# Optimization experiments

Measured on AMD Instinct MI355X. Metric: run time of the kernel, lower is better.

Reference implementation:

```python
import jax, jax.numpy as jnp
import numpy as np

ATT_WIDTH = 512  # attention_width from init

def _band_mask(T, width, dtype):
    # tf.matrix_band_part(ones, width//2, (width-1)//2): keep i-j<=lower and j-i<=upper
    lower = width // 2
    upper = (width - 1) // 2
    i = jnp.arange(T)[:, None]
    j = jnp.arange(T)[None, :]
    keep = (i - j <= lower) & (j - i <= upper)
    return keep.astype(dtype)

def setup_inputs() -> dict:
    key = jax.random.key(0)
    k1, k2, k3, k4 = jax.random.split(key, 4)
    B, T, H, D = 8, 2048, 1024, 1024
    scale = 1.0 / np.sqrt(H)  # keep activations sane
    return {
        "inputs": jax.random.normal(k1, (B, T, H), dtype=jnp.float32),
        "WQ": jax.random.normal(k2, (H, D), dtype=jnp.float32) * scale,
        "WK": jax.random.normal(k3, (H, D), dtype=jnp.float32) * scale,
        "WV": jax.random.normal(k4, (H, D), dtype=jnp.float32) * scale,
    }

def reference(inputs, WQ, WK, WV) -> jnp.ndarray:
    B, T, H = inputs.shape
    D = WQ.shape[1]
    scale = jnp.asarray(D, inputs.dtype) ** 0.5
    q = jnp.einsum('bth,hd->btd', inputs, WQ)
    k = jnp.einsum('bth,hd->btd', inputs, WK)
    v = jnp.einsum('bth,hd->btd', inputs, WV)
    score = jnp.einsum('bqd,bkd->bqk', q, k) / scale  # [B,T,T]
    # NOTE: original multiplies score by the 0/1 band mask BEFORE softmax
    # (masked entries become 0, not -inf). Faithful reproduction.
    local = _band_mask(T, ATT_WIDTH, score.dtype)
    score = score * local[None, :, :]
    attn = jax.nn.softmax(score, axis=-1)
    return jnp.einsum('bqk,bkd->bqd', attn, v)
```

## Files before the change

kernel.cpp:

```cpp
#include <hip/hip_runtime.h>
#include <hip/hip_bf16.h>
#include <stdint.h>

typedef __attribute__((ext_vector_type(8))) short bf16x8;
typedef __attribute__((ext_vector_type(4))) short short4v;
typedef __attribute__((ext_vector_type(4))) float f32x4;

#define DEV static __device__ __forceinline__

DEV float bf2f(short u) {
    union { float f; uint32_t i; } c; c.i = ((uint32_t)(uint16_t)u) << 16; return c.f;
}
DEV short f2bf(float f) {
    union { float f; uint32_t i; } c; c.f = f;
    uint32_t i = c.i;
    uint32_t r = i + 0x7FFFu + ((i >> 16) & 1u);
    return (short)(r >> 16);
}

DEV void gload_lds16(const short* g, short* l) {
    __builtin_amdgcn_global_load_lds(
        (const __attribute__((address_space(1))) void*)g,
        (__attribute__((address_space(3))) void*)l,
        16, 0, 0);
}

__global__ __launch_bounds__(256)
void cvt_f32_bf16(const float* __restrict__ in, short* __restrict__ out) {
    long i = ((long)blockIdx.x * 256 + threadIdx.x) * 8;
    float4 a = *(const float4*)&in[i];
    float4 b = *(const float4*)&in[i + 4];
    bf16x8 o;
    o[0] = f2bf(a.x); o[1] = f2bf(a.y); o[2] = f2bf(a.z); o[3] = f2bf(a.w);
    o[4] = f2bf(b.x); o[5] = f2bf(b.y); o[6] = f2bf(b.z); o[7] = f2bf(b.w);
    *(bf16x8*)&out[i] = o;
}

__global__ __launch_bounds__(256)
void transpose_w(const float* __restrict__ W, short* __restrict__ Wt) {
    const int HD = 1024;
    __shared__ float tile[32][33];
    int bx = blockIdx.x, by = blockIdx.y;
    int tx = threadIdx.x & 31, ty = threadIdx.x >> 5;
    #pragma unroll
    for (int r = ty; r < 32; r += 8)
        tile[r][tx] = W[(long)(by * 32 + r) * HD + bx * 32 + tx];
    __syncthreads();
    #pragma unroll
    for (int r = ty; r < 32; r += 8)
        Wt[(long)(bx * 32 + r) * HD + by * 32 + tx] = f2bf(tile[tx][r]);
}


DEV void stage_half(const short* __restrict__ src, int ld, short* dst, int tid) {
    int rr = tid >> 3;
    int cs = ((tid & 7) ^ (rr & 7)) << 3;
    short* d = dst + ((tid >> 6) << 9);
    gload_lds16(src + (long)rr * ld + cs, d);
    gload_lds16(src + (long)(rr + 64) * ld + cs, d + 4096);
}

DEV bf16x8 ld_frag(const short* half, int rowbase, int ks, int lane) {
    int row = rowbase + (lane & 15);
    int idx = (row << 6) + ks * 32 + ((lane >> 4) << 3);
    idx ^= (lane & 7) << 3;
    return *(const bf16x8*)&half[idx];
}

#define SCHED0 __builtin_amdgcn_sched_barrier(0)
#define SBAR do { SCHED0; __builtin_amdgcn_s_barrier(); SCHED0; } while (0)
#define LGK(n) do { asm volatile("s_waitcnt lgkmcnt(" #n ")" ::: "memory"); SCHED0; } while (0)
#define VM(n)  do { asm volatile("s_waitcnt vmcnt(" #n ")" ::: "memory"); SCHED0; } while (0)
#define PRIO1 __builtin_amdgcn_s_setprio(1)
#define PRIO0 __builtin_amdgcn_s_setprio(0)

#define READ_A(HP, QM)                                                          \
    do { _Pragma("unroll") for (int iq = 0; iq < 4; ++iq)                       \
         _Pragma("unroll") for (int ks = 0; ks < 2; ++ks)                       \
             ra[iq][ks] = ld_frag(HP, (QM)*64 + iq*16, ks, lane); } while (0)

#define READ_B(HP, QN)                                                          \
    do { _Pragma("unroll") for (int jn = 0; jn < 2; ++jn)                       \
         _Pragma("unroll") for (int ks = 0; ks < 2; ++ks)                       \
             rb[QN][jn][ks] = ld_frag(HP, wn1*64 + (QN)*32 + jn*16, ks, lane); } while (0)

#define MFMA_Q(QM, QN)                                                          \
    do { _Pragma("unroll") for (int iq = 0; iq < 4; ++iq)                       \
         _Pragma("unroll") for (int jn = 0; jn < 2; ++jn)                       \
         _Pragma("unroll") for (int ks = 0; ks < 2; ++ks)                       \
             acc[(QM)*4+iq][(QN)*2+jn] = __builtin_amdgcn_mfma_f32_16x16x32_bf16( \
                 ra[iq][ks], rb[QN][jn][ks], acc[(QM)*4+iq][(QN)*2+jn], 0,0,0); } while (0)

template<int EPI>
__global__ __launch_bounds__(512, 2)
void gemm256(const short* __restrict__ Abase, const short* __restrict__ Bbase,
             void* __restrict__ o0, void* __restrict__ o1, void* __restrict__ o2,
             const float* __restrict__ Crow, const float* __restrict__ Vsum)
{
    const int T = 2048, HD = 1024;
    __shared__ __align__(16) short lds[2][2][2][8192];

    const int tid  = threadIdx.x;
    const int lane = tid & 63;
    const int w    = tid >> 6;
    const int wm   = w >> 2;
    const int wn   = w & 3;
    const int wn1  = wn & 1;

    int m0, n0, klo, khi, ldA, ldB, bz;
    const short *A, *B;
    if (EPI == 0) {
        int p = (int)blockIdx.x + 12 * (int)blockIdx.y;
        int lid = (p & 7) * 96 + (p >> 3);
        m0 = (lid / 12) * 256; n0 = (lid % 12) * 256;
        klo = 0; khi = 1024; ldA = HD; ldB = HD; bz = 0;
        A = Abase; B = Bbase;
    } else if (EPI == 1) {
        int p = (int)blockIdx.x + 3 * ((int)blockIdx.y + 8 * (int)blockIdx.z);
        bz = p & 7; int rem = p >> 3;
        int mb = rem / 3, kb = mb + rem % 3 - 1;
        if (kb < 0 || kb > 7) return;
        m0 = mb * 256; n0 = kb * 256;
        klo = 0; khi = 1024; ldA = HD; ldB = HD;
        A = Abase + (long)bz * T * HD; B = Bbase + (long)bz * T * HD;
    } else {
        int p = (int)blockIdx.x + 4 * ((int)blockIdx.y + 8 * (int)blockIdx.z);
        bz = p & 7; int rem = p >> 3;
        int mb = rem / 4;
        m0 = mb * 256; n0 = (rem % 4) * 256;
        klo = max(m0 - 256, 0); khi = min(m0 + 512, T);
        ldA = T; ldB = T;
        A = Abase + (long)bz * T * T; B = Bbase + (long)bz * HD * T;
    }

    const short* Asrc = A + (long)m0 * ldA + klo;
    const short* Bsrc = B + (long)n0 * ldB + klo;
    const short* hA0 = &lds[0][0][wm][0];
    const short* hA1 = &lds[1][0][wm][0];
    const short* hB0 = &lds[0][1][wn >> 1][0];
    const short* hB1 = &lds[1][1][wn >> 1][0];

    auto stA = [&](int bf, int hf, int t) {
        stage_half(Asrc + (long)hf * 128 * ldA + t * 64, ldA, (short*)&lds[bf][0][hf][0], tid); };
    auto stB = [&](int bf, int hf, int t) {
        stage_half(Bsrc + (long)hf * 128 * ldB + t * 64, ldB, (short*)&lds[bf][1][hf][0], tid); };

    f32x4 acc[8][4];
    #pragma unroll
    for (int i = 0; i < 8; ++i)
        #pragma unroll
        for (int j = 0; j < 4; ++j) { acc[i][j][0]=0.f; acc[i][j][1]=0.f; acc[i][j][2]=0.f; acc[i][j][3]=0.f; }
    bf16x8 ra[4][2];
    bf16x8 rb[2][2][2];

    const int NT = (khi - klo) >> 6;

    stB(0,0,0); stB(0,1,0); stA(0,0,0); stA(0,1,0); stB(1,0,1); stB(1,1,1);
    SCHED0; VM(4); SBAR;
    READ_B(hB0, 0); SCHED0;

    #pragma unroll 1
    for (int i = 0; i < NT/2 - 1; ++i) {
        int t1 = 2*i+1, t2 = 2*i+2, t3 = 2*i+3;
        SBAR; READ_A(hA0,0); SCHED0; READ_B(hB0,1); SCHED0; stA(1,0,t1);
        LGK(4); PRIO1; MFMA_Q(0,0); PRIO0; SCHED0;
        SBAR; stA(1,1,t1); LGK(0); PRIO1; MFMA_Q(0,1); PRIO0; SCHED0;
        SBAR; READ_A(hA0,1); SCHED0; stB(0,0,t2); LGK(0);
        PRIO1; MFMA_Q(1,0); PRIO0; SCHED0; VM(2); SCHED0;
        SBAR; READ_B(hB1,0); SCHED0; stB(0,1,t2);
        PRIO1; MFMA_Q(1,1); PRIO0; SCHED0;
        SBAR; READ_A(hA1,0); SCHED0; READ_B(hB1,1); SCHED0; stA(0,0,t2);
        LGK(4); PRIO1; MFMA_Q(0,0); PRIO0; SCHED0;
        SBAR; stA(0,1,t2); LGK(0); PRIO1; MFMA_Q(0,1); PRIO0; SCHED0;
        SBAR; READ_A(hA1,1); SCHED0; stB(1,0,t3); LGK(0);
        PRIO1; MFMA_Q(1,0); PRIO0; SCHED0; VM(2); SCHED0;
        SBAR; READ_B(hB0,0); SCHED0; stB(1,1,t3);
        PRIO1; MFMA_Q(1,1); PRIO0; SCHED0;
    }
    {
        int t1 = NT - 1;
        SBAR; READ_A(hA0,0); SCHED0; READ_B(hB0,1); SCHED0; stA(1,0,t1);
        LGK(4); PRIO1; MFMA_Q(0,0); PRIO0; SCHED0;
        SBAR; stA(1,1,t1); LGK(0); PRIO1; MFMA_Q(0,1); PRIO0; SCHED0;
        SBAR; READ_A(hA0,1); SCHED0; LGK(0);
        PRIO1; MFMA_Q(1,0); PRIO0; SCHED0; VM(0); SCHED0;
        SBAR; READ_B(hB1,0); SCHED0; PRIO1; MFMA_Q(1,1); PRIO0; SCHED0;
        SBAR; READ_A(hA1,0); SCHED0; READ_B(hB1,1); SCHED0;
        LGK(4); PRIO1; MFMA_Q(0,0); PRIO0; SCHED0;
        SBAR; LGK(0); PRIO1; MFMA_Q(0,1); PRIO0; SCHED0;
        SBAR; READ_A(hA1,1); SCHED0; LGK(0); PRIO1; MFMA_Q(1,0); PRIO0; SCHED0;
        SBAR; PRIO1; MFMA_Q(1,1); PRIO0; SCHED0;
    }

    const int fr = lane & 15, fq = lane >> 4;
    const int rbase = m0 + wm * 128, cbase = n0 + wn * 64;

    if (EPI == 0) {
        const int wsel = n0 >> 10;
        if (wsel < 2) {
            short* dst = (short*)(wsel ? o1 : o0);
            #pragma unroll
            for (int mi = 0; mi < 8; ++mi)
                #pragma unroll
                for (int ni = 0; ni < 4; ++ni)
                    #pragma unroll
                    for (int r = 0; r < 4; ++r) {
                        int row = rbase + mi * 16 + fq * 4 + r;
                        int col = (cbase + ni * 16 + fr) & 1023;
                        dst[(long)row * HD + col] = f2bf(acc[mi][ni][r]);
                    }
        } else {
            short* Vt = (short*)o2;
            #pragma unroll
            for (int mi = 0; mi < 8; ++mi)
                #pragma unroll
                for (int ni = 0; ni < 4; ++ni) {
                    int col  = (cbase + ni * 16 + fr) & 1023;
                    int row0 = rbase + mi * 16 + fq * 4;
                    int b = row0 >> 11, t = row0 & 2047;
                    short4v v;
                    #pragma unroll
                    for (int r = 0; r < 4; ++r) v[r] = f2bf(acc[mi][ni][r]);
                    *(short4v*)&Vt[((long)b * HD + col) * T + t] = v;
                }
        }
    } else if (EPI == 1) {
        short* S = (short*)o0 + (long)bz * T * T;
        #pragma unroll
        for (int mi = 0; mi < 8; ++mi)
            #pragma unroll
            for (int ni = 0; ni < 4; ++ni)
                #pragma unroll
                for (int r = 0; r < 4; ++r) {
                    int i = rbase + mi * 16 + fq * 4 + r;
                    int j = cbase + ni * 16 + fr;
                    bool keep = (i - j <= 256) && (j - i <= 255);
                    S[(long)i * T + j] = f2bf(keep ? acc[mi][ni][r] * (1.f/32.f) : 0.f);
                }
    } else {
        float* out = (float*)o0;
        #pragma unroll
        for (int mi = 0; mi < 8; ++mi)
            #pragma unroll
            for (int r = 0; r < 4; ++r) {
                int i = rbase + mi * 16 + fq * 4 + r;
                float ci = Crow[bz * T + i];
                #pragma unroll
                for (int ni = 0; ni < 4; ++ni) {
                    int col = cbase + ni * 16 + fr;
                    out[((long)bz * T + i) * HD + col] = acc[mi][ni][r] + ci * Vsum[bz * HD + col];
                }
            }
    }
}

__global__ __launch_bounds__(256)
void softmax_band(short* __restrict__ S, float* __restrict__ Crow) {
    const int T = 2048;
    int wid = (int)blockIdx.x * 4 + (threadIdx.x >> 6);
    int lane = threadIdx.x & 63;
    int b = wid >> 11, t = wid & 2047;
    int mb = t >> 7;
    int tlo = max(mb - 2, 0) * 128;
    int thi = min(mb + 2, 15) * 128 + 128;
    int nvec = (thi - tlo) >> 3;
    short* row = S + ((long)b * T + t) * T + tlo;

    bool h0 = lane < nvec;
    bool h1 = lane + 64 < nvec;
    bf16x8 v0, v1;
    float f0[8], f1[8];
    float m = 0.f;
    if (h0) {
        v0 = *(const bf16x8*)&row[lane * 8];
        #pragma unroll
        for (int j = 0; j < 8; ++j) { f0[j] = bf2f(v0[j]); m = fmaxf(m, f0[j]); }
    }
    if (h1) {
        v1 = *(const bf16x8*)&row[(lane + 64) * 8];
        #pragma unroll
        for (int j = 0; j < 8; ++j) { f1[j] = bf2f(v1[j]); m = fmaxf(m, f1[j]); }
    }
    #pragma unroll
    for (int o = 32; o; o >>= 1) m = fmaxf(m, __shfl_xor(m, o));

    float e0[8], e1[8];
    float sum = 0.f;
    if (h0) {
        #pragma unroll
        for (int j = 0; j < 8; ++j) { e0[j] = __expf(f0[j] - m); sum += e0[j]; }
    }
    if (h1) {
        #pragma unroll
        for (int j = 0; j < 8; ++j) { e1[j] = __expf(f1[j] - m); sum += e1[j]; }
    }
    #pragma unroll
    for (int o = 32; o; o >>= 1) sum += __shfl_xor(sum, o);
    float em = __expf(-m);
    sum += (float)(2048 - nvec * 8) * em;
    float inv = 1.f / sum;
    float c = em * inv;

    if (h0) {
        #pragma unroll
        for (int j = 0; j < 8; ++j) v0[j] = f2bf(e0[j] * inv - c);
        *(bf16x8*)&row[lane * 8] = v0;
    }
    if (h1) {
        #pragma unroll
        for (int j = 0; j < 8; ++j) v1[j] = f2bf(e1[j] * inv - c);
        *(bf16x8*)&row[(lane + 64) * 8] = v1;
    }
    if (lane == 0) Crow[wid] = c;
}

__global__ __launch_bounds__(256)
void vsum_rows(const short* __restrict__ Vt, float* __restrict__ Vsum) {
    int rowid = (int)blockIdx.x * 4 + (threadIdx.x >> 6);
    int lane = threadIdx.x & 63;
    const short* r = Vt + (long)rowid * 2048;
    float s = 0.f;
    #pragma unroll
    for (int v = 0; v < 4; ++v) {
        bf16x8 x = *(const bf16x8*)&r[(lane + v * 64) * 8];
        #pragma unroll
        for (int j = 0; j < 8; ++j) s += bf2f(x[j]);
    }
    #pragma unroll
    for (int o = 32; o; o >>= 1) s += __shfl_xor(s, o);
    if (lane == 0) Vsum[rowid] = s;
}

extern "C" void kernel_launch(void* const* d_in, const int* in_sizes, int n_in,
                              void* d_out, int out_size, void* d_ws, size_t ws_size,
                              hipStream_t stream) {
    const int B = 8, T = 2048, H = 1024, D = 1024;
    const long MT = (long)B * T;

    const float* X  = (const float*)d_in[0];
    const float* WQ = (const float*)d_in[1];
    const float* WK = (const float*)d_in[2];
    const float* WV = (const float*)d_in[3];
    float* out = (float*)d_out;

    char* ws = (char*)d_ws;
    size_t off = 0;
    auto alloc = [&](size_t bytes) {
        char* p = ws + off;
        off += (bytes + 255) & ~(size_t)255;
        return p;
    };
    short* Xb   = (short*)alloc(MT * H * 2);
    short* Wt   = (short*)alloc(3L * D * H * 2);
    short* Qb   = (short*)alloc(MT * D * 2);
    short* Kb   = (short*)alloc(MT * D * 2);
    short* Vt   = (short*)alloc((long)B * D * T * 2);
    short* S    = (short*)alloc((long)B * T * T * 2);
    float* Crow = (float*)alloc(MT * 4);
    float* Vsum = (float*)alloc((long)B * D * 4);
    if (off > ws_size) return;

    cvt_f32_bf16<<<(int)(MT * H / 2048), 256, 0, stream>>>(X, Xb);
    transpose_w<<<dim3(32, 32), 256, 0, stream>>>(WQ, Wt);
    transpose_w<<<dim3(32, 32), 256, 0, stream>>>(WK, Wt + (long)D * H);
    transpose_w<<<dim3(32, 32), 256, 0, stream>>>(WV, Wt + 2L * D * H);

    gemm256<0><<<dim3(12, 64, 1), 512, 0, stream>>>(Xb, Wt, Qb, Kb, Vt, nullptr, nullptr);

    vsum_rows<<<(int)(B * D / 4), 256, 0, stream>>>(Vt, Vsum);

    gemm256<1><<<dim3(3, 8, B), 512, 0, stream>>>(Qb, Kb, S, nullptr, nullptr, nullptr, nullptr);

    softmax_band<<<(int)(MT / 4), 256, 0, stream>>>(S, Crow);

    gemm256<2><<<dim3(4, 8, B), 512, 0, stream>>>(S, Vt, out, nullptr, nullptr, Crow, Vsum);
}
```

Baseline: 236.9 us.

## Fold WQ·WKᵀ into one matrix so scores use X directly instead of K

```diff
diff --git a/kernel.cpp b/kernel.cpp
--- a/kernel.cpp
+++ b/kernel.cpp
@@ -51,6 +51,26 @@
         Wt[(long)(bx * 32 + r) * HD + by * 32 + tx] = f2bf(tile[tx][r]);
 }
 
+__global__ __launch_bounds__(256)
+void reduce_mt(const float* __restrict__ Mpart, short* __restrict__ MTb) {
+    const long SL = 1024L * 1024;
+    long i = ((long)blockIdx.x * 256 + threadIdx.x) * 8;
+    float s[8];
+    #pragma unroll
+    for (int j = 0; j < 8; ++j) s[j] = 0.f;
+    #pragma unroll
+    for (int sl = 0; sl < 4; ++sl) {
+        float4 a = *(const float4*)&Mpart[sl * SL + i];
+        float4 b = *(const float4*)&Mpart[sl * SL + i + 4];
+        s[0] += a.x; s[1] += a.y; s[2] += a.z; s[3] += a.w;
+        s[4] += b.x; s[5] += b.y; s[6] += b.z; s[7] += b.w;
+    }
+    bf16x8 o;
+    #pragma unroll
+    for (int j = 0; j < 8; ++j) o[j] = f2bf(s[j]);
+    *(bf16x8*)&MTb[i] = o;
+}
+
 
 DEV void stage_half(const short* __restrict__ src, int ld, short* dst, int tid) {
     int rr = tid >> 3;
@@ -110,9 +130,9 @@
     int m0, n0, klo, khi, ldA, ldB, bz;
     const short *A, *B;
     if (EPI == 0) {
-        int p = (int)blockIdx.x + 12 * (int)blockIdx.y;
-        int lid = (p & 7) * 96 + (p >> 3);
-        m0 = (lid / 12) * 256; n0 = (lid % 12) * 256;
+        int p = (int)blockIdx.x + 8 * (int)blockIdx.y;
+        int lid = (p & 7) * 64 + (p >> 3);
+        m0 = (lid >> 3) * 256; n0 = (lid & 7) * 256;
         klo = 0; khi = 1024; ldA = HD; ldB = HD; bz = 0;
         A = Abase; B = Bbase;
     } else if (EPI == 1) {
@@ -123,7 +143,7 @@
         m0 = mb * 256; n0 = kb * 256;
         klo = 0; khi = 1024; ldA = HD; ldB = HD;
         A = Abase + (long)bz * T * HD; B = Bbase + (long)bz * T * HD;
-    } else {
+    } else if (EPI == 2) {
         int p = (int)blockIdx.x + 4 * ((int)blockIdx.y + 8 * (int)blockIdx.z);
         bz = p & 7; int rem = p >> 3;
         int mb = rem / 4;
@@ -131,6 +151,11 @@
         klo = max(m0 - 256, 0); khi = min(m0 + 512, T);
         ldA = T; ldB = T;
         A = Abase + (long)bz * T * T; B = Bbase + (long)bz * HD * T;
+    } else {
+        m0 = blockIdx.y * 256; n0 = blockIdx.x * 256;
+        klo = (int)blockIdx.z * 256; khi = klo + 256;
+        ldA = HD; ldB = HD; bz = 0;
+        A = Abase; B = Bbase;
     }
 
     const short* Asrc = A + (long)m0 * ldA + klo;
@@ -197,8 +222,8 @@
 
     if (EPI == 0) {
         const int wsel = n0 >> 10;
-        if (wsel < 2) {
-            short* dst = (short*)(wsel ? o1 : o0);
+        if (wsel == 0) {
+            short* dst = (short*)o0;
             #pragma unroll
             for (int mi = 0; mi < 8; ++mi)
                 #pragma unroll
@@ -206,7 +231,7 @@
                     #pragma unroll
                     for (int r = 0; r < 4; ++r) {
                         int row = rbase + mi * 16 + fq * 4 + r;
-                        int col = (cbase + ni * 16 + fr) & 1023;
+                        int col = cbase + ni * 16 + fr;
                         dst[(long)row * HD + col] = f2bf(acc[mi][ni][r]);
                     }
         } else {
@@ -237,7 +262,7 @@
                     bool keep = (i - j <= 256) && (j - i <= 255);
                     S[(long)i * T + j] = f2bf(keep ? acc[mi][ni][r] * (1.f/32.f) : 0.f);
                 }
-    } else {
+    } else if (EPI == 2) {
         float* out = (float*)o0;
         #pragma unroll
         for (int mi = 0; mi < 8; ++mi)
@@ -251,6 +276,18 @@
                     out[((long)bz * T + i) * HD + col] = acc[mi][ni][r] + ci * Vsum[bz * HD + col];
                 }
             }
+    } else {
+        float* dst = (float*)o0 + (long)blockIdx.z * HD * HD;
+        #pragma unroll
+        for (int mi = 0; mi < 8; ++mi)
+            #pragma unroll
+            for (int ni = 0; ni < 4; ++ni)
+                #pragma unroll
+                for (int r = 0; r < 4; ++r) {
+                    int row = rbase + mi * 16 + fq * 4 + r;
+                    int col = cbase + ni * 16 + fr;
+                    dst[(long)row * HD + col] = acc[mi][ni][r];
+                }
     }
 }
 
@@ -350,26 +387,33 @@
         off += (bytes + 255) & ~(size_t)255;
         return p;
     };
-    short* Xb   = (short*)alloc(MT * H * 2);
-    short* Wt   = (short*)alloc(3L * D * H * 2);
-    short* Qb   = (short*)alloc(MT * D * 2);
-    short* Kb   = (short*)alloc(MT * D * 2);
-    short* Vt   = (short*)alloc((long)B * D * T * 2);
-    short* S    = (short*)alloc((long)B * T * T * 2);
-    float* Crow = (float*)alloc(MT * 4);
-    float* Vsum = (float*)alloc((long)B * D * 4);
+    short* Xb    = (short*)alloc(MT * H * 2);
+    short* WQb   = (short*)alloc((long)H * D * 2);
+    short* WKb   = (short*)alloc((long)H * D * 2);
+    short* Bfuse = (short*)alloc(2L * D * H * 2);
+    short* MTb   = Bfuse;
+    short* WVt   = Bfuse + (long)D * H;
+    float* Mpart = (float*)alloc(4L * D * H * 4);
+    short* Gb    = (short*)alloc(MT * D * 2);
+    short* Vt    = (short*)alloc((long)B * D * T * 2);
+    short* S     = (short*)alloc((long)B * T * T * 2);
+    float* Crow  = (float*)alloc(MT * 4);
+    float* Vsum  = (float*)alloc((long)B * D * 4);
     if (off > ws_size) return;
 
     cvt_f32_bf16<<<(int)(MT * H / 2048), 256, 0, stream>>>(X, Xb);
-    transpose_w<<<dim3(32, 32), 256, 0, stream>>>(WQ, Wt);
-    transpose_w<<<dim3(32, 32), 256, 0, stream>>>(WK, Wt + (long)D * H);
-    transpose_w<<<dim3(32, 32), 256, 0, stream>>>(WV, Wt + 2L * D * H);
-
-    gemm256<0><<<dim3(12, 64, 1), 512, 0, stream>>>(Xb, Wt, Qb, Kb, Vt, nullptr, nullptr);
+    cvt_f32_bf16<<<512, 256, 0, stream>>>(WQ, WQb);
+    cvt_f32_bf16<<<512, 256, 0, stream>>>(WK, WKb);
+    transpose_w<<<dim3(32, 32), 256, 0, stream>>>(WV, WVt);
+
+    gemm256<3><<<dim3(4, 4, 4), 512, 0, stream>>>(WKb, WQb, Mpart, nullptr, nullptr, nullptr, nullptr);
+    reduce_mt<<<512, 256, 0, stream>>>(Mpart, MTb);
+
+    gemm256<0><<<dim3(8, 64, 1), 512, 0, stream>>>(Xb, Bfuse, Gb, nullptr, Vt, nullptr, nullptr);
 
     vsum_rows<<<(int)(B * D / 4), 256, 0, stream>>>(Vt, Vsum);
 
-    gemm256<1><<<dim3(3, 8, B), 512, 0, stream>>>(Qb, Kb, S, nullptr, nullptr, nullptr, nullptr);
+    gemm256<1><<<dim3(3, 8, B), 512, 0, stream>>>(Gb, Xb, S, nullptr, nullptr, nullptr, nullptr);
 
     softmax_band<<<(int)(MT / 4), 256, 0, stream>>>(S, Crow);
 
```

Result: faster. 212.5 us (-10.3%).
